# Kernel tuning notes

Measured on AMD Instinct MI355X. Metric: run time of the kernel, lower is better.

Reference implementation:

```python
import jax, jax.numpy as jnp
import numpy as np

N_NODES = 50000
N_EDGES = 800000
IN_FEATS = 128
HIDDEN = 256
N_CLASSES = 64


def setup_inputs() -> dict:
    key = jax.random.key(0)
    ks = jax.random.split(key, 16)
    def w(k, shape, fan_in):
        return jax.random.normal(k, shape, dtype=jnp.float32) * (1.0 / np.sqrt(fan_in))
    inp = {
        "x": jax.random.normal(ks[0], (N_NODES, IN_FEATS), dtype=jnp.float32),
        "edge_src": jax.random.randint(ks[1], (N_EDGES,), 0, N_NODES, dtype=jnp.int32),
        "edge_dst": jax.random.randint(ks[2], (N_EDGES,), 0, N_NODES, dtype=jnp.int32),
        # layer 0: in_feats -> hidden
        "W0s": w(ks[3], (IN_FEATS, HIDDEN), IN_FEATS),
        "W0n": w(ks[4], (IN_FEATS, HIDDEN), IN_FEATS),
        "b0": jnp.zeros((HIDDEN,), dtype=jnp.float32),
        # layer 1: hidden -> hidden
        "W1s": w(ks[5], (HIDDEN, HIDDEN), HIDDEN),
        "W1n": w(ks[6], (HIDDEN, HIDDEN), HIDDEN),
        "b1": jnp.zeros((HIDDEN,), dtype=jnp.float32),
        # layer 2: hidden -> hidden (last conv also outputs hidden per source code)
        "W2s": w(ks[7], (HIDDEN, HIDDEN), HIDDEN),
        "W2n": w(ks[8], (HIDDEN, HIDDEN), HIDDEN),
        "b2": jnp.zeros((HIDDEN,), dtype=jnp.float32),
        # fc1: hidden -> n_classes
        "Wfc": w(ks[9], (HIDDEN, N_CLASSES), HIDDEN),
        "bfc": jnp.zeros((N_CLASSES,), dtype=jnp.float32),
    }
    return inp


def _sage_layer(h, src, dst, Ws, Wn, b):
    # mean-neighbor aggregation: segment-sum messages, divide by in-degree
    msg = h[src]  # [E, D] irregular gather
    agg = jax.ops.segment_sum(msg, dst, num_segments=N_NODES)  # [N, D]
    deg = jax.ops.segment_sum(jnp.ones_like(dst, dtype=h.dtype), dst, num_segments=N_NODES)
    h_neigh = agg / jnp.maximum(deg, 1.0)[:, None]
    # DGL SAGEConv (mean): fc_self(h) + fc_neigh(h_neigh) + bias
    return h @ Ws + h_neigh @ Wn + b


def reference(x, edge_src, edge_dst, W0s, W0n, b0, W1s, W1n, b1, W2s, W2n, b2, Wfc, bfc):
    # forward applies dropout (identity at eval) and NO activation between layers,
    # matching the original module's forward().
    h = _sage_layer(x, edge_src, edge_dst, W0s, W0n, b0)
    h = _sage_layer(h, edge_src, edge_dst, W1s, W1n, b1)
    h = _sage_layer(h, edge_src, edge_dst, W2s, W2n, b2)
    return h @ Wfc + bfc  # [N, n_classes]
```

## Files before the change

kernel.cpp:

```cpp
#include <hip/hip_runtime.h>

#define NN 50000
#define NE 800000
#define F_IN 128
#define HID 256
#define N_CLS 64
#define SCAN_BLOCKS ((NN + 255) / 256)
#define HEPT 4
#define HB2 ((NE + 256 * HEPT - 1) / (256 * HEPT))
#define CF_BLOCKS 36
#define CL_BLOCKS 9
#define GA_BLOCKS ((NN + 127) / 128)
#define CROWS 515

typedef _Float16 half8 __attribute__((ext_vector_type(8)));
typedef float f32x4 __attribute__((ext_vector_type(4)));

__device__ __forceinline__ const float* virtC1_row(int r, const float* W0s,
                                                   const float* W0n, const float* b0) {
    if (r < 0) return nullptr;
    if (r < 128) return W0s + (size_t)r * 256;
    if (r < 256) return W0n + (size_t)(r - 128) * 256;
    if (r == 512) return b0;
    return nullptr;
}

__device__ __forceinline__ int shift_src(int r) {
    if (r >= 128 && r < 512) return r - 128;
    if (r == 513) return 512;
    if (r == 514) return 513;
    return -1;
}

__device__ __forceinline__ void compose_first_dev(
    int bx, const float* __restrict__ W0s, const float* __restrict__ W0n,
    const float* __restrict__ b0,
    const float* __restrict__ B1, const float* __restrict__ B2,
    const float* __restrict__ brow, float* __restrict__ C)
{
    __shared__ float As[64][17];
    __shared__ float Bs[16][64];
    const int tid = threadIdx.x;
    const int tx = tid & 15, ty = tid >> 4;
    const int row0 = (bx % 9) * 64;
    const int col0 = (bx / 9) * 64;
    const int lr = tid >> 2, lc = tid & 3;
    const int br = tid >> 4, bc = tid & 15;

    const int grow = row0 + lr;
    const int srcr0 = (grow < CROWS) ? grow : -1;
    const float* ap0 = virtC1_row(srcr0, W0s, W0n, b0);
    const float* ap1 = virtC1_row(shift_src(grow), W0s, W0n, b0);

    float acc[4][4] = {};

    float4 av = ap0 ? *(const float4*)(ap0 + lc * 4) : make_float4(0.f, 0.f, 0.f, 0.f);
    float4 bv = *(const float4*)(B1 + (size_t)br * 256 + col0 + bc * 4);

    for (int s = 0; s < 32; ++s) {
        As[lr][lc * 4 + 0] = av.x;
        As[lr][lc * 4 + 1] = av.y;
        As[lr][lc * 4 + 2] = av.z;
        As[lr][lc * 4 + 3] = av.w;
        *(float4*)&Bs[br][bc * 4] = bv;
        __syncthreads();
        if (s + 1 < 32) {
            int pass = (s + 1) >> 4;
            int k0 = ((s + 1) & 15) << 4;
            const float* ap = pass ? ap1 : ap0;
            const float* B = pass ? B2 : B1;
            av = ap ? *(const float4*)(ap + k0 + lc * 4) : make_float4(0.f, 0.f, 0.f, 0.f);
            bv = *(const float4*)(B + (size_t)(k0 + br) * 256 + col0 + bc * 4);
        }
        #pragma unroll
        for (int k = 0; k < 16; ++k) {
            float a[4];
            #pragma unroll
            for (int i = 0; i < 4; ++i) a[i] = As[ty * 4 + i][k];
            float4 bb = *(const float4*)&Bs[k][tx * 4];
            const float b[4] = {bb.x, bb.y, bb.z, bb.w};
            #pragma unroll
            for (int i = 0; i < 4; ++i)
                #pragma unroll
                for (int j = 0; j < 4; ++j)
                    acc[i][j] += a[i] * b[j];
        }
        __syncthreads();
    }

    #pragma unroll
    for (int i = 0; i < 4; ++i) {
        int r = row0 + ty * 4 + i;
        if (r < CROWS) {
            #pragma unroll
            for (int j = 0; j < 4; ++j) {
                float v = acc[i][j];
                if (r == 512) v += brow[col0 + tx * 4 + j];
                C[(size_t)r * 256 + col0 + tx * 4 + j] = v;
            }
        }
    }
}

__device__ __forceinline__ void compose_mid_dev(
    int bx, const float* __restrict__ A,
    const float* __restrict__ B1, const float* __restrict__ B2,
    const float* __restrict__ brow, float* __restrict__ C)
{
    __shared__ float As[64][17];
    __shared__ float Bs[16][64];
    const int tid = threadIdx.x;
    const int tx = tid & 15, ty = tid >> 4;
    const int row0 = (bx % 9) * 64;
    const int col0 = (bx / 9) * 64;
    const int lr = tid >> 2, lc = tid & 3;
    const int br = tid >> 4, bc = tid & 15;

    const int grow = row0 + lr;
    const int p0 = (grow < CROWS) ? grow : -1;
    const int p1 = shift_src(grow);

    float acc[4][4] = {};

    float4 av = (p0 >= 0) ? *(const float4*)(A + (size_t)p0 * 256 + lc * 4)
                          : make_float4(0.f, 0.f, 0.f, 0.f);
    float4 bv = *(const float4*)(B1 + (size_t)br * 256 + col0 + bc * 4);

    for (int s = 0; s < 32; ++s) {
        As[lr][lc * 4 + 0] = av.x;
        As[lr][lc * 4 + 1] = av.y;
        As[lr][lc * 4 + 2] = av.z;
        As[lr][lc * 4 + 3] = av.w;
        *(float4*)&Bs[br][bc * 4] = bv;
        __syncthreads();
        if (s + 1 < 32) {
            int pass = (s + 1) >> 4;
            int k0 = ((s + 1) & 15) << 4;
            int p = pass ? p1 : p0;
            const float* B = pass ? B2 : B1;
            av = (p >= 0) ? *(const float4*)(A + (size_t)p * 256 + k0 + lc * 4)
                          : make_float4(0.f, 0.f, 0.f, 0.f);
            bv = *(const float4*)(B + (size_t)(k0 + br) * 256 + col0 + bc * 4);
        }
        #pragma unroll
        for (int k = 0; k < 16; ++k) {
            float a[4];
            #pragma unroll
            for (int i = 0; i < 4; ++i) a[i] = As[ty * 4 + i][k];
            float4 bb = *(const float4*)&Bs[k][tx * 4];
            const float b[4] = {bb.x, bb.y, bb.z, bb.w};
            #pragma unroll
            for (int i = 0; i < 4; ++i)
                #pragma unroll
                for (int j = 0; j < 4; ++j)
                    acc[i][j] += a[i] * b[j];
        }
        __syncthreads();
    }

    #pragma unroll
    for (int i = 0; i < 4; ++i) {
        int r = row0 + ty * 4 + i;
        if (r < CROWS) {
            #pragma unroll
            for (int j = 0; j < 4; ++j) {
                float v = acc[i][j];
                if (r == 512) v += brow[col0 + tx * 4 + j];
                C[(size_t)r * 256 + col0 + tx * 4 + j] = v;
            }
        }
    }
}

__device__ __forceinline__ void compose_last_dev(
    int bx, const float* __restrict__ A, const float* __restrict__ B1,
    const float* __restrict__ brow, float* __restrict__ Vf, _Float16* __restrict__ BT)
{
    __shared__ float As[64][17];
    __shared__ float Bs[16][64];
    const int tid = threadIdx.x;
    const int tx = tid & 15, ty = tid >> 4;
    const int row0 = bx * 64;
    const int lr = tid >> 2, lc = tid & 3;
    const int br = tid >> 4, bc = tid & 15;

    const int grow = row0 + lr;
    const float* ap = (grow < CROWS) ? (A + (size_t)grow * 256) : nullptr;

    float acc[4][4] = {};

    float4 av = ap ? *(const float4*)(ap + lc * 4) : make_float4(0.f, 0.f, 0.f, 0.f);
    float4 bv = *(const float4*)(B1 + (size_t)br * 64 + bc * 4);

    for (int s = 0; s < 16; ++s) {
        As[lr][lc * 4 + 0] = av.x;
        As[lr][lc * 4 + 1] = av.y;
        As[lr][lc * 4 + 2] = av.z;
        As[lr][lc * 4 + 3] = av.w;
        *(float4*)&Bs[br][bc * 4] = bv;
        __syncthreads();
        if (s + 1 < 16) {
            int k0 = (s + 1) << 4;
            av = ap ? *(const float4*)(ap + k0 + lc * 4) : make_float4(0.f, 0.f, 0.f, 0.f);
            bv = *(const float4*)(B1 + (size_t)(k0 + br) * 64 + bc * 4);
        }
        #pragma unroll
        for (int k = 0; k < 16; ++k) {
            float a[4];
            #pragma unroll
            for (int i = 0; i < 4; ++i) a[i] = As[ty * 4 + i][k];
            float4 bb = *(const float4*)&Bs[k][tx * 4];
            const float b[4] = {bb.x, bb.y, bb.z, bb.w};
            #pragma unroll
            for (int i = 0; i < 4; ++i)
                #pragma unroll
                for (int j = 0; j < 4; ++j)
                    acc[i][j] += a[i] * b[j];
        }
        __syncthreads();
    }

    #pragma unroll
    for (int i = 0; i < 4; ++i) {
        int r = row0 + ty * 4 + i;
        if (r < CROWS) {
            #pragma unroll
            for (int j = 0; j < 4; ++j) {
                int c = tx * 4 + j;
                float v = acc[i][j];
                if (r == 512) v += brow[c];
                Vf[(size_t)r * 64 + c] = v;
                if (r < 512)
                    BT[(size_t)((r >> 7) * 64 + c) * 128 + (r & 127)] = (_Float16)v;
            }
        }
    }
}

__device__ __forceinline__ void scan_block_sums_dev(const int* __restrict__ cnt,
                                                    int* __restrict__ blockSums, int n, int bx) {
    __shared__ int s[256];
    int t = threadIdx.x;
    int i = bx * 256 + t;
    s[t] = (i < n) ? cnt[i] : 0;
    __syncthreads();
    for (int off = 128; off > 0; off >>= 1) {
        if (t < off) s[t] += s[t + off];
        __syncthreads();
    }
    if (t == 0) blockSums[bx] = s[0];
}

__device__ __forceinline__ void scan_top_dev(int* __restrict__ blockSums, int nb) {
    __shared__ int s[256];
    int t = threadIdx.x;
    s[t] = (t < nb) ? blockSums[t] : 0;
    __syncthreads();
    for (int off = 1; off < 256; off <<= 1) {
        int v = (t >= off) ? s[t - off] : 0;
        __syncthreads();
        s[t] += v;
        __syncthreads();
    }
    if (t < nb) blockSums[t] = (t > 0) ? s[t - 1] : 0;
}

__device__ __forceinline__ void scan_final_dev(const int* __restrict__ cnt,
                                               const int* __restrict__ blockBase,
                                               int* __restrict__ offs,
                                               float* __restrict__ dinv, int n, int bx) {
    __shared__ int s[256];
    int t = threadIdx.x;
    int i = bx * 256 + t;
    int v = (i < n) ? cnt[i] : 0;
    s[t] = v;
    __syncthreads();
    for (int off = 1; off < 256; off <<= 1) {
        int u = (t >= off) ? s[t - off] : 0;
        __syncthreads();
        s[t] += u;
        __syncthreads();
    }
    if (i < n) {
        offs[i] = blockBase[bx] + s[t] - v;
        dinv[i] = 1.0f / (float)max(v, 1);
    }
    if (i == n - 1) offs[n] = blockBase[bx] + s[t];
}

__device__ __forceinline__ void gemm_y_dev(
    int bx, int by,
    const float* __restrict__ X, const _Float16* __restrict__ BT,
    _Float16* __restrict__ Y, _Float16* __restrict__ Tc, int N)
{
    constexpr int LP = 40;
    __shared__ _Float16 As[128 * LP];
    __shared__ _Float16 Bs[128 * LP];

    const int tid = threadIdx.x;
    const int wave = tid >> 6;
    const int lane = tid & 63;
    const int l15 = lane & 15;
    const int quad = lane >> 4;
    const int wrow = wave >> 1;
    const int wcol = wave & 1;
    const int m_base = wrow * 64;
    const int n_base = wcol * 64;

    const int row0 = bx * 128;
    const int col0 = by * 128;

    f32x4 acc[4][4] = {};

    for (int k0 = 0; k0 < 128; k0 += 32) {
        #pragma unroll
        for (int r = 0; r < 2; ++r) {
            int idx = r * 256 + tid;
            int row = idx >> 2, ch = idx & 3;
            int gr = row0 + row; if (gr > N - 1) gr = N - 1;
            const float* ap = X + (size_t)gr * 128 + k0 + ch * 8;
            float4 f0 = *(const float4*)ap;
            float4 f1 = *(const float4*)(ap + 4);
            half8 v = { (_Float16)f0.x, (_Float16)f0.y, (_Float16)f0.z, (_Float16)f0.w,
                        (_Float16)f1.x, (_Float16)f1.y, (_Float16)f1.z, (_Float16)f1.w };
            *(half8*)&As[row * LP + ch * 8] = v;
        }
        #pragma unroll
        for (int r = 0; r < 2; ++r) {
            int idx = r * 256 + tid;
            int row = idx >> 2, ch = idx & 3;
            *(half8*)&Bs[row * LP + ch * 8] =
                *(const half8*)(BT + (size_t)(col0 + row) * 128 + k0 + ch * 8);
        }
        __syncthreads();
        half8 af[4], bf[4];
        #pragma unroll
        for (int i = 0; i < 4; ++i)
            af[i] = *(const half8*)&As[(m_base + i * 16 + l15) * LP + quad * 8];
        #pragma unroll
        for (int j = 0; j < 4; ++j)
            bf[j] = *(const half8*)&Bs[(n_base + j * 16 + l15) * LP + quad * 8];
        #pragma unroll
        for (int i = 0; i < 4; ++i)
            #pragma unroll
            for (int j = 0; j < 4; ++j)
                acc[i][j] = __builtin_amdgcn_mfma_f32_16x16x32_f16(af[i], bf[j], acc[i][j], 0, 0, 0);
        __syncthreads();
    }

    #pragma unroll
    for (int i = 0; i < 4; ++i) {
        #pragma unroll
        for (int j = 0; j < 4; ++j) {
            int col = col0 + n_base + j * 16 + l15;
            #pragma unroll
            for (int r = 0; r < 4; ++r) {
                int row = row0 + m_base + i * 16 + quad * 4 + r;
                if (row < N) {
                    _Float16 v = (_Float16)acc[i][j][r];
                    Y[(size_t)row * 256 + col] = v;
                    if (col >= 192) Tc[(size_t)row * 64 + (col - 192)] = v;
                }
            }
        }
    }
}

__global__ __launch_bounds__(256) void k_composeF_hist(
    const int* __restrict__ edst, int* __restrict__ cnt, unsigned short* __restrict__ rank,
    const float* __restrict__ W0s, const float* __restrict__ W0n, const float* __restrict__ b0,
    const float* __restrict__ W1s, const float* __restrict__ W1n, const float* __restrict__ b1,
    float* __restrict__ C2)
{
    if (blockIdx.x < CF_BLOCKS) {
        compose_first_dev(blockIdx.x, W0s, W0n, b0, W1s, W1n, b1, C2);
    } else {
        int base = (blockIdx.x - CF_BLOCKS) * (256 * HEPT) + threadIdx.x;
        int d[HEPT];
        #pragma unroll
        for (int k = 0; k < HEPT; ++k) {
            int e = base + k * 256;
            d[k] = (e < NE) ? edst[e] : -1;
        }
        #pragma unroll
        for (int k = 0; k < HEPT; ++k) {
            int e = base + k * 256;
            if (d[k] >= 0) rank[e] = (unsigned short)atomicAdd(&cnt[d[k]], 1);
        }
    }
}

__global__ __launch_bounds__(256) void k_composeM_scanA(
    const int* __restrict__ cnt, int* __restrict__ blockSums,
    const float* __restrict__ C2,
    const float* __restrict__ W2s, const float* __restrict__ W2n, const float* __restrict__ b2,
    float* __restrict__ C3)
{
    if (blockIdx.x < CF_BLOCKS) compose_mid_dev(blockIdx.x, C2, W2s, W2n, b2, C3);
    else scan_block_sums_dev(cnt, blockSums, NN, blockIdx.x - CF_BLOCKS);
}

__global__ __launch_bounds__(256) void k_scanT_composeL(
    int* __restrict__ blockSums,
    const float* __restrict__ C3, const float* __restrict__ Wfc, const float* __restrict__ bfc,
    float* __restrict__ Vf, _Float16* __restrict__ BT)
{
    if (blockIdx.x == 0) scan_top_dev(blockSums, SCAN_BLOCKS);
    else compose_last_dev(blockIdx.x - 1, C3, Wfc, bfc, Vf, BT);
}

__global__ __launch_bounds__(256) void k_gemmA_scanF(
    const int* __restrict__ cnt, const int* __restrict__ blockBase,
    int* __restrict__ offs, float* __restrict__ dinv,
    const float* __restrict__ X, const _Float16* __restrict__ BT,
    _Float16* __restrict__ Y, _Float16* __restrict__ Tc)
{
    if (blockIdx.x < GA_BLOCKS) gemm_y_dev(blockIdx.x, 0, X, BT, Y, Tc, NN);
    else scan_final_dev(cnt, blockBase, offs, dinv, NN, blockIdx.x - GA_BLOCKS);
}

__global__ __launch_bounds__(256) void k_gemmB_place(
    const int* __restrict__ esrc, const int* __restrict__ edst,
    const unsigned short* __restrict__ rank, const int* __restrict__ offs,
    unsigned short* __restrict__ csr,
    const float* __restrict__ X, const _Float16* __restrict__ BT,
    _Float16* __restrict__ Y, _Float16* __restrict__ Tc)
{
    if (blockIdx.x < GA_BLOCKS) {
        gemm_y_dev(blockIdx.x, 1, X, BT, Y, Tc, NN);
    } else {
        int base = (blockIdx.x - GA_BLOCKS) * (256 * HEPT) + threadIdx.x;
        int d[HEPT], s[HEPT], r[HEPT];
        #pragma unroll
        for (int k = 0; k < HEPT; ++k) {
            int e = base + k * 256;
            if (e < NE) { d[k] = edst[e]; s[k] = esrc[e]; r[k] = rank[e]; }
            else d[k] = -1;
        }
        #pragma unroll
        for (int k = 0; k < HEPT; ++k) {
            if (d[k] >= 0) csr[offs[d[k]] + r[k]] = (unsigned short)s[k];
        }
    }
}

template <bool OUT_F32>
__global__ __launch_bounds__(256) void gather64(
    const _Float16* __restrict__ Tin,
    const unsigned short* __restrict__ csr, const int* __restrict__ offs,
    const float* __restrict__ dinv,
    const _Float16* __restrict__ Yadd,
    const float* __restrict__ cvec,
    void* __restrict__ Tout, int N)
{
    int node = blockIdx.x * 32 + (threadIdx.x >> 3);
    int lane = threadIdx.x & 7;
    if (node >= N) return;
    int beg = offs[node], end = offs[node + 1];
    float acc[8] = {};
    int e = beg;
    for (; e + 7 < end; e += 8) {
        int s0 = csr[e], s1 = csr[e + 1], s2 = csr[e + 2], s3 = csr[e + 3];
        int s4 = csr[e + 4], s5 = csr[e + 5], s6 = csr[e + 6], s7 = csr[e + 7];
        half8 v0 = *(const half8*)(Tin + (size_t)s0 * 64 + lane * 8);
        half8 v1 = *(const half8*)(Tin + (size_t)s1 * 64 + lane * 8);
        half8 v2 = *(const half8*)(Tin + (size_t)s2 * 64 + lane * 8);
        half8 v3 = *(const half8*)(Tin + (size_t)s3 * 64 + lane * 8);
        half8 v4 = *(const half8*)(Tin + (size_t)s4 * 64 + lane * 8);
        half8 v5 = *(const half8*)(Tin + (size_t)s5 * 64 + lane * 8);
        half8 v6 = *(const half8*)(Tin + (size_t)s6 * 64 + lane * 8);
        half8 v7 = *(const half8*)(Tin + (size_t)s7 * 64 + lane * 8);
        #pragma unroll
        for (int j = 0; j < 8; ++j)
            acc[j] += (((float)v0[j] + (float)v1[j]) + ((float)v2[j] + (float)v3[j]))
                    + (((float)v4[j] + (float)v5[j]) + ((float)v6[j] + (float)v7[j]));
    }
    for (; e + 3 < end; e += 4) {
        int s0 = csr[e], s1 = csr[e + 1], s2 = csr[e + 2], s3 = csr[e + 3];
        half8 v0 = *(const half8*)(Tin + (size_t)s0 * 64 + lane * 8);
        half8 v1 = *(const half8*)(Tin + (size_t)s1 * 64 + lane * 8);
        half8 v2 = *(const half8*)(Tin + (size_t)s2 * 64 + lane * 8);
        half8 v3 = *(const half8*)(Tin + (size_t)s3 * 64 + lane * 8);
        #pragma unroll
        for (int j = 0; j < 8; ++j)
            acc[j] += ((float)v0[j] + (float)v1[j]) + ((float)v2[j] + (float)v3[j]);
    }
    for (; e < end; ++e) {
        half8 v = *(const half8*)(Tin + (size_t)csr[e] * 64 + lane * 8);
        #pragma unroll
        for (int j = 0; j < 8; ++j) acc[j] += (float)v[j];
    }
    float sc = dinv[node];
    half8 y = *(const half8*)(Yadd + (size_t)node * 256 + lane * 8);
    if (OUT_F32) {
        float* o = (float*)Tout + (size_t)node * 64 + lane * 8;
        float4 o0, o1;
        o0.x = acc[0] * sc + (float)y[0] + cvec[lane * 8 + 0];
        o0.y = acc[1] * sc + (float)y[1] + cvec[lane * 8 + 1];
        o0.z = acc[2] * sc + (float)y[2] + cvec[lane * 8 + 2];
        o0.w = acc[3] * sc + (float)y[3] + cvec[lane * 8 + 3];
        o1.x = acc[4] * sc + (float)y[4] + cvec[lane * 8 + 4];
        o1.y = acc[5] * sc + (float)y[5] + cvec[lane * 8 + 5];
        o1.z = acc[6] * sc + (float)y[6] + cvec[lane * 8 + 6];
        o1.w = acc[7] * sc + (float)y[7] + cvec[lane * 8 + 7];
        *(float4*)o = o0;
        *(float4*)(o + 4) = o1;
    } else {
        half8 o;
        #pragma unroll
        for (int j = 0; j < 8; ++j)
            o[j] = (_Float16)(acc[j] * sc + (float)y[j] + cvec[lane * 8 + j]);
        *(half8*)((_Float16*)Tout + (size_t)node * 64 + lane * 8) = o;
    }
}

extern "C" void kernel_launch(void* const* d_in, const int* in_sizes, int n_in,
                              void* d_out, int out_size, void* d_ws, size_t ws_size,
                              hipStream_t stream) {
    const float* x    = (const float*)d_in[0];
    const int*   esrc = (const int*)d_in[1];
    const int*   edst = (const int*)d_in[2];
    const float* W0s  = (const float*)d_in[3];
    const float* W0n  = (const float*)d_in[4];
    const float* b0   = (const float*)d_in[5];
    const float* W1s  = (const float*)d_in[6];
    const float* W1n  = (const float*)d_in[7];
    const float* b1   = (const float*)d_in[8];
    const float* W2s  = (const float*)d_in[9];
    const float* W2n  = (const float*)d_in[10];
    const float* b2   = (const float*)d_in[11];
    const float* Wfc  = (const float*)d_in[12];
    const float* bfc  = (const float*)d_in[13];
    float* out = (float*)d_out;

    _Float16* Y   = (_Float16*)d_ws;
    _Float16* Ta  = Y + (size_t)NN * 256;
    _Float16* Tb  = Ta + (size_t)NN * 64;
    _Float16* Tc  = Tb + (size_t)NN * 64;
    _Float16* BT  = Tc + (size_t)NN * 64;
    float* C2     = (float*)(BT + 256 * 128);
    float* C3     = C2 + CROWS * 256;
    float* Vf     = C3 + CROWS * 256;
    float* dinv   = Vf + CROWS * 64;
    int* cnt      = (int*)(dinv + NN);
    int* offs     = cnt + NN;
    int* blockSums = offs + NN + 1;
    unsigned short* rank = (unsigned short*)(blockSums + SCAN_BLOCKS);
    unsigned short* csr  = rank + NE;

    hipMemsetAsync(cnt, 0, (size_t)NN * sizeof(int), stream);

    k_composeF_hist<<<CF_BLOCKS + HB2, 256, 0, stream>>>(
        edst, cnt, rank, W0s, W0n, b0, W1s, W1n, b1, C2);

    k_composeM_scanA<<<CF_BLOCKS + SCAN_BLOCKS, 256, 0, stream>>>(
        cnt, blockSums, C2, W2s, W2n, b2, C3);

    k_scanT_composeL<<<1 + CL_BLOCKS, 256, 0, stream>>>(
        blockSums, C3, Wfc, bfc, Vf, BT);

    k_gemmA_scanF<<<GA_BLOCKS + SCAN_BLOCKS, 256, 0, stream>>>(
        cnt, blockSums, offs, dinv, x, BT, Y, Tc);

    k_gemmB_place<<<GA_BLOCKS + HB2, 256, 0, stream>>>(
        esrc, edst, rank, offs, csr, x, BT, Y, Tc);

    const int ggrid = (NN + 31) / 32;
    gather64<false><<<ggrid, 256, 0, stream>>>(
        Tc, csr, offs, dinv, Y + 128, Vf + (size_t)514 * 64, (void*)Ta, NN);
    gather64<false><<<ggrid, 256, 0, stream>>>(
        Ta, csr, offs, dinv, Y + 64, Vf + (size_t)513 * 64, (void*)Tb, NN);
    gather64<true><<<ggrid, 256, 0, stream>>>(
        Tb, csr, offs, dinv, Y, Vf + (size_t)512 * 64, (void*)out, NN);
}
```

Measured before the change: 265.6 us.

## Split edge histogram across compose kernels and fold top scan into final scan

```diff
diff --git a/kernel.cpp b/kernel.cpp
--- a/kernel.cpp
+++ b/kernel.cpp
@@ -2,12 +2,14 @@
 
 #define NN 50000
 #define NE 800000
+#define NE_HALF 400000
 #define F_IN 128
 #define HID 256
 #define N_CLS 64
 #define SCAN_BLOCKS ((NN + 255) / 256)
 #define HEPT 4
 #define HB2 ((NE + 256 * HEPT - 1) / (256 * HEPT))
+#define HBH ((NE_HALF + 256 * HEPT - 1) / (256 * HEPT))
 #define CF_BLOCKS 36
 #define CL_BLOCKS 9
 #define GA_BLOCKS ((NN + 127) / 128)
@@ -234,6 +236,25 @@
                     BT[(size_t)((r >> 7) * 64 + c) * 128 + (r & 127)] = (_Float16)v;
             }
         }
+    }
+}
+
+__device__ __forceinline__ void hist_dev(int bx, int start, int count,
+                                         const int* __restrict__ edst,
+                                         int* __restrict__ cnt,
+                                         unsigned short* __restrict__ rank) {
+    int base = start + bx * (256 * HEPT) + threadIdx.x;
+    int lim = start + count;
+    int d[HEPT];
+    #pragma unroll
+    for (int k = 0; k < HEPT; ++k) {
+        int e = base + k * 256;
+        d[k] = (e < lim) ? edst[e] : -1;
+    }
+    #pragma unroll
+    for (int k = 0; k < HEPT; ++k) {
+        int e = base + k * 256;
+        if (d[k] >= 0) rank[e] = (unsigned short)atomicAdd(&cnt[d[k]], 1);
     }
 }
 
@@ -251,10 +272,14 @@
     if (t == 0) blockSums[bx] = s[0];
 }
 
-__device__ __forceinline__ void scan_top_dev(int* __restrict__ blockSums, int nb) {
+__device__ __forceinline__ void scan_final2_dev(const int* __restrict__ cnt,
+                                                const int* __restrict__ blockSums,
+                                                int* __restrict__ offs,
+                                                float* __restrict__ dinv, int n, int bx) {
     __shared__ int s[256];
+    __shared__ int base_sh;
     int t = threadIdx.x;
-    s[t] = (t < nb) ? blockSums[t] : 0;
+    s[t] = (t < SCAN_BLOCKS) ? blockSums[t] : 0;
     __syncthreads();
     for (int off = 1; off < 256; off <<= 1) {
         int v = (t >= off) ? s[t - off] : 0;
@@ -262,15 +287,10 @@
         s[t] += v;
         __syncthreads();
     }
-    if (t < nb) blockSums[t] = (t > 0) ? s[t - 1] : 0;
-}
-
-__device__ __forceinline__ void scan_final_dev(const int* __restrict__ cnt,
-                                               const int* __restrict__ blockBase,
-                                               int* __restrict__ offs,
-                                               float* __restrict__ dinv, int n, int bx) {
-    __shared__ int s[256];
-    int t = threadIdx.x;
+    if (t == 0) base_sh = (bx > 0) ? s[bx - 1] : 0;
+    __syncthreads();
+    int base = base_sh;
+    __syncthreads();
     int i = bx * 256 + t;
     int v = (i < n) ? cnt[i] : 0;
     s[t] = v;
@@ -282,10 +302,10 @@
         __syncthreads();
     }
     if (i < n) {
-        offs[i] = blockBase[bx] + s[t] - v;
+        offs[i] = base + s[t] - v;
         dinv[i] = 1.0f / (float)max(v, 1);
     }
-    if (i == n - 1) offs[n] = blockBase[bx] + s[t];
+    if (i == n - 1) offs[n] = base + s[t];
 }
 
 __device__ __forceinline__ void gemm_y_dev(
@@ -375,48 +395,37 @@
     if (blockIdx.x < CF_BLOCKS) {
         compose_first_dev(blockIdx.x, W0s, W0n, b0, W1s, W1n, b1, C2);
     } else {
-        int base = (blockIdx.x - CF_BLOCKS) * (256 * HEPT) + threadIdx.x;
-        int d[HEPT];
-        #pragma unroll
-        for (int k = 0; k < HEPT; ++k) {
-            int e = base + k * 256;
-            d[k] = (e < NE) ? edst[e] : -1;
-        }
-        #pragma unroll
-        for (int k = 0; k < HEPT; ++k) {
-            int e = base + k * 256;
-            if (d[k] >= 0) rank[e] = (unsigned short)atomicAdd(&cnt[d[k]], 1);
-        }
-    }
-}
-
-__global__ __launch_bounds__(256) void k_composeM_scanA(
-    const int* __restrict__ cnt, int* __restrict__ blockSums,
+        hist_dev(blockIdx.x - CF_BLOCKS, 0, NE_HALF, edst, cnt, rank);
+    }
+}
+
+__global__ __launch_bounds__(256) void k_composeM_hist2(
+    const int* __restrict__ edst, int* __restrict__ cnt, unsigned short* __restrict__ rank,
     const float* __restrict__ C2,
     const float* __restrict__ W2s, const float* __restrict__ W2n, const float* __restrict__ b2,
     float* __restrict__ C3)
 {
     if (blockIdx.x < CF_BLOCKS) compose_mid_dev(blockIdx.x, C2, W2s, W2n, b2, C3);
-    else scan_block_sums_dev(cnt, blockSums, NN, blockIdx.x - CF_BLOCKS);
-}
-
-__global__ __launch_bounds__(256) void k_scanT_composeL(
-    int* __restrict__ blockSums,
+    else hist_dev(blockIdx.x - CF_BLOCKS, NE_HALF, NE - NE_HALF, edst, cnt, rank);
+}
+
+__global__ __launch_bounds__(256) void k_composeL_scanA(
+    const int* __restrict__ cnt, int* __restrict__ blockSums,
     const float* __restrict__ C3, const float* __restrict__ Wfc, const float* __restrict__ bfc,
     float* __restrict__ Vf, _Float16* __restrict__ BT)
 {
-    if (blockIdx.x == 0) scan_top_dev(blockSums, SCAN_BLOCKS);
-    else compose_last_dev(blockIdx.x - 1, C3, Wfc, bfc, Vf, BT);
+    if (blockIdx.x < CL_BLOCKS) compose_last_dev(blockIdx.x, C3, Wfc, bfc, Vf, BT);
+    else scan_block_sums_dev(cnt, blockSums, NN, blockIdx.x - CL_BLOCKS);
 }
 
 __global__ __launch_bounds__(256) void k_gemmA_scanF(
-    const int* __restrict__ cnt, const int* __restrict__ blockBase,
+    const int* __restrict__ cnt, const int* __restrict__ blockSums,
     int* __restrict__ offs, float* __restrict__ dinv,
     const float* __restrict__ X, const _Float16* __restrict__ BT,
     _Float16* __restrict__ Y, _Float16* __restrict__ Tc)
 {
     if (blockIdx.x < GA_BLOCKS) gemm_y_dev(blockIdx.x, 0, X, BT, Y, Tc, NN);
-    else scan_final_dev(cnt, blockBase, offs, dinv, NN, blockIdx.x - GA_BLOCKS);
+    else scan_final2_dev(cnt, blockSums, offs, dinv, NN, blockIdx.x - GA_BLOCKS);
 }
 
 __global__ __launch_bounds__(256) void k_gemmB_place(
@@ -550,14 +559,14 @@
 
     hipMemsetAsync(cnt, 0, (size_t)NN * sizeof(int), stream);
 
-    k_composeF_hist<<<CF_BLOCKS + HB2, 256, 0, stream>>>(
+    k_composeF_hist<<<CF_BLOCKS + HBH, 256, 0, stream>>>(
         edst, cnt, rank, W0s, W0n, b0, W1s, W1n, b1, C2);
 
-    k_composeM_scanA<<<CF_BLOCKS + SCAN_BLOCKS, 256, 0, stream>>>(
-        cnt, blockSums, C2, W2s, W2n, b2, C3);
-
-    k_scanT_composeL<<<1 + CL_BLOCKS, 256, 0, stream>>>(
-        blockSums, C3, Wfc, bfc, Vf, BT);
+    k_composeM_hist2<<<CF_BLOCKS + HBH, 256, 0, stream>>>(
+        edst, cnt, rank, C2, W2s, W2n, b2, C3);
+
+    k_composeL_scanA<<<CL_BLOCKS + SCAN_BLOCKS, 256, 0, stream>>>(
+        cnt, blockSums, C3, Wfc, bfc, Vf, BT);
 
     k_gemmA_scanF<<<GA_BLOCKS + SCAN_BLOCKS, 256, 0, stream>>>(
         cnt, blockSums, offs, dinv, x, BT, Y, Tc);
```

Result: faster. 260.3 us (-2.0%).
